# Kernel tuning notes

Hardware: AMD Instinct MI355X
Metric: run time of the kernel (lower is better)

The kernel has to match this reference:

```python
import jax, jax.numpy as jnp
import numpy as np
from jax import lax


def _bilinear_gather(img, ys, xs):
    """img: [B,H,W,C]; ys,xs: [B,K,H,W] fractional coords. Zero padding outside.
    Returns [B,K,H,W,C]."""
    B, H, W, C = img.shape
    y0 = jnp.floor(ys)
    x0 = jnp.floor(xs)
    wy = (ys - y0)[..., None]
    wx = (xs - x0)[..., None]
    y0i = y0.astype(jnp.int32)
    x0i = x0.astype(jnp.int32)
    flat = img.reshape(B, H * W, C)

    def gather(yi, xi):
        valid = (yi >= 0) & (yi < H) & (xi >= 0) & (xi < W)
        yc = jnp.clip(yi, 0, H - 1)
        xc = jnp.clip(xi, 0, W - 1)
        idx = (yc * W + xc).reshape(B, -1, 1)
        g = jnp.take_along_axis(flat, idx, axis=1).reshape(yi.shape + (C,))
        return g * valid[..., None].astype(img.dtype)

    v00 = gather(y0i, x0i)
    v01 = gather(y0i, x0i + 1)
    v10 = gather(y0i + 1, x0i)
    v11 = gather(y0i + 1, x0i + 1)
    one = jnp.asarray(1.0, img.dtype)
    return (v00 * (one - wy) * (one - wx) + v01 * (one - wy) * wx
            + v10 * wy * (one - wx) + v11 * wy * wx)


def _forward(x, w_off, b_off, w_def, b_def, w_attn, b_attn):
    B, Cin, H, W = x.shape
    Cout = w_def.shape[0]
    # offset conv: 3x3, pad 1 -> [B, 18, H, W]
    off = lax.conv_general_dilated(x, w_off, (1, 1), ((1, 1), (1, 1)))
    off = off + b_off[None, :, None, None]
    off = off.reshape(B, 9, 2, H, W)
    dy = off[:, :, 0]  # [B,9,H,W], torchvision order: (dy, dx) per kernel pt
    dx = off[:, :, 1]
    # kernel point grid, row-major over (kh, kw)
    ky, kx = jnp.meshgrid(jnp.arange(3), jnp.arange(3), indexing='ij')
    ky = ky.reshape(9).astype(x.dtype)
    kx = kx.reshape(9).astype(x.dtype)
    ii = jnp.arange(H, dtype=x.dtype)
    jj = jnp.arange(W, dtype=x.dtype)
    # sample position = (out_pos - pad + k) + offset, pad=1, stride=1
    ys = ii[None, None, :, None] - 1.0 + ky[None, :, None, None] + dy
    xs = jj[None, None, None, :] - 1.0 + kx[None, :, None, None] + dx
    img = x.transpose(0, 2, 3, 1)  # [B,H,W,Cin]
    sampled = _bilinear_gather(img, ys, xs)  # [B,9,H,W,Cin]
    wk = w_def.reshape(Cout, Cin, 9)  # row-major kernel pts match ky/kx
    out = jnp.einsum('bkhwc,ock->bohw', sampled, wk) + b_def[None, :, None, None]
    # spatial attention: 1x1 conv -> sigmoid gate
    attn = jnp.einsum('bchw,oc->bohw', out, w_attn[:, :, 0, 0]) + b_attn[None, :, None, None]
    out = out * jax.nn.sigmoid(attn)
    return jax.nn.relu(out)


def setup_inputs() -> dict:
    key = jax.random.key(0)
    ks = jax.random.split(key, 5)
    B, C, H, W = 4, 128, 128, 128
    x = jax.random.normal(ks[0], (B, C, H, W), dtype=jnp.float32)
    w_off = jax.random.normal(ks[1], (18, C, 3, 3), dtype=jnp.float32) * 0.02
    b_off = jnp.zeros((18,), dtype=jnp.float32)
    w_def = jax.random.normal(ks[2], (C, C, 3, 3), dtype=jnp.float32) * (1.0 / np.sqrt(C * 9))
    b_def = jnp.zeros((C,), dtype=jnp.float32)
    w_attn = jax.random.normal(ks[3], (1, C, 1, 1), dtype=jnp.float32) * (1.0 / np.sqrt(C))
    b_attn = jnp.zeros((1,), dtype=jnp.float32)
    return {"x": x, "w_off": w_off, "b_off": b_off, "w_def": w_def,
            "b_def": b_def, "w_attn": w_attn, "b_attn": b_attn}


def reference(x, w_off, b_off, w_def, b_def, w_attn, b_attn):
    return _forward(x, w_off, b_off, w_def, b_def, w_attn, b_attn)
```

## Files before the change

### kernel.cpp

```cpp
#include <hip/hip_runtime.h>
#include <math.h>

#define Cch 128
#define Hh 128
#define Ww 128
#define HW (Hh * Ww)

typedef __attribute__((ext_vector_type(8))) short short8;
typedef __attribute__((ext_vector_type(4))) float float4v;
typedef __attribute__((ext_vector_type(2))) float float2v;
typedef __attribute__((ext_vector_type(4))) unsigned int uint4v;

__device__ __forceinline__ unsigned short f2bf(float f) {
    unsigned u = __float_as_uint(f);
    return (unsigned short)((u + 0x8000u) >> 16);
}
__device__ __forceinline__ float2v up2(unsigned u) {
    return (float2v){__uint_as_float(u << 16), __uint_as_float(u & 0xffff0000u)};
}
__device__ __forceinline__ unsigned packbf2(float lo, float hi) {
    unsigned a = __float_as_uint(lo), b = __float_as_uint(hi);
    return ((a + 0x8000u) >> 16) | ((b + 0x8000u) & 0xffff0000u);
}

__global__ __launch_bounds__(256) void pack_x_v3(const float* __restrict__ x,
                                                 unsigned short* __restrict__ xt) {
    __shared__ unsigned int tile[64][68];
    int t   = threadIdx.x;
    int blk = blockIdx.x;
    int b   = blk >> 8;
    int p0  = (blk & 255) << 6;
    const float* xb = x + (size_t)b * Cch * HW + p0;

    int c2i = t >> 4;
    int q   = t & 15;
    #pragma unroll
    for (int it = 0; it < 4; ++it) {
        int c2 = it * 16 + c2i;
        int px = q * 4;
        float4v a = *(const float4v*)&xb[(size_t)(2 * c2) * HW + px];
        float4v c = *(const float4v*)&xb[(size_t)(2 * c2 + 1) * HW + px];
        #pragma unroll
        for (int j = 0; j < 4; ++j)
            tile[px + j][c2] = packbf2(a[j], c[j]);
    }
    __syncthreads();
    unsigned short* xtb = xt + (size_t)b * HW * Cch + (size_t)p0 * Cch;
    int g  = t & 15;
    int pw = t >> 4;
    #pragma unroll
    for (int it = 0; it < 4; ++it) {
        int p = pw + 16 * it;
        uint4v v = *(const uint4v*)&tile[p][g * 4];
        *(uint4v*)(xtb + (size_t)p * Cch + g * 8) = v;
    }
}

#define NFB (9 * 4 * 8 * 64 * 8)
#define NFO (9 * 4 * 2 * 64 * 8)
__global__ __launch_bounds__(256) void build_frags(const float* __restrict__ w_def,
                                                   const float* __restrict__ w_off,
                                                   unsigned short* __restrict__ wfB,
                                                   unsigned short* __restrict__ wfO) {
    int idx = blockIdx.x * 256 + threadIdx.x;
    if (idx < NFB) {
        int j = idx & 7, lane = (idx >> 3) & 63, t = (idx >> 9) & 7;
        int q = (idx >> 12) & 3, k = idx >> 14;
        int c = 32 * q + 8 * (lane >> 4) + j;
        int o = 16 * t + (lane & 15);
        wfB[idx] = f2bf(w_def[(size_t)(o * Cch + c) * 9 + k]);
    } else if (idx < NFB + NFO) {
        int i2 = idx - NFB;
        int j = i2 & 7, lane = (i2 >> 3) & 63, t = (i2 >> 9) & 1;
        int q = (i2 >> 10) & 3, k = i2 >> 12;
        int c = 32 * q + 8 * (lane >> 4) + j;
        int o = 16 * t + (lane & 15);
        wfO[i2] = (o < 18) ? f2bf(w_off[(size_t)(o * Cch + c) * 9 + k]) : (unsigned short)0;
    }
}

__device__ __forceinline__ void blk_map(int blk, int& b, int& h, int& w0) {
    int xcd = blk & 7;
    b = xcd >> 1;
    int seg = ((xcd & 1) << 8) | (blk >> 3);
    h  = seg >> 2;
    w0 = (seg & 3) << 5;
}

__global__ __launch_bounds__(128, 2) void fused_srt(const unsigned short* __restrict__ xt,
                                                    const unsigned short* __restrict__ wfB,
                                                    const unsigned short* __restrict__ wfO,
                                                    const float* __restrict__ b_off,
                                                    const float* __restrict__ b_def,
                                                    const float* __restrict__ w_attn,
                                                    const float* __restrict__ b_attn,
                                                    float* __restrict__ out) {
    __shared__ float4v red[2 * 8 * 64];
    __shared__ float   offs[32 * 18];
    __shared__ uint4v  smw[2 * 4 * 64];
    int b, h, w0;
    blk_map(blockIdx.x, b, h, w0);
    int tid  = threadIdx.x;
    int wave = tid >> 6;
    int lane = tid & 63;
    int col  = lane & 15;
    int s    = lane >> 4;
    int spx  = lane >> 2;
    int sch  = lane & 3;
    int cbase = 64 * wave;
    int csrt  = cbase + sch * 8;
    int wbase = wave * 256;
    int rIdx  = wbase + ((lane & 15) * 4 + (lane >> 4));

    const unsigned short* xtb = xt + (size_t)b * HW * Cch;

    {
        float4v acc2[2][2];
        #pragma unroll
        for (int pt = 0; pt < 2; ++pt)
            #pragma unroll
            for (int t = 0; t < 2; ++t) {
                int o = 16 * t + col;
                float bv = (wave == 0 && o < 18) ? b_off[o] : 0.0f;
                acc2[pt][t] = (float4v){bv, bv, bv, bv};
            }

        #pragma unroll
        for (int k = 0; k < 9; ++k) {
            int y = h + (k / 3) - 1;
            bool vy = (y >= 0) && (y < Hh);
            int yc = min(max(y, 0), Hh - 1);
            int dxk = (k % 3) - 1;
            int  ofs[2];
            bool val[2];
            #pragma unroll
            for (int pt = 0; pt < 2; ++pt) {
                int px = w0 + 16 * pt + spx;
                int xs = px + dxk;
                val[pt] = vy && (xs >= 0) && (xs < Ww);
                int xc  = min(max(xs, 0), Ww - 1);
                ofs[pt] = (yc * Ww + xc) * Cch + csrt;
            }
            #pragma unroll
            for (int pt = 0; pt < 2; ++pt)
                #pragma unroll
                for (int qq = 0; qq < 2; ++qq) {
                    uint4v av = *(const uint4v*)(xtb + ofs[pt] + 32 * qq);
                    if (!val[pt]) av = (uint4v){0u, 0u, 0u, 0u};
                    smw[wbase + (pt * 2 + qq) * 64 + lane] = av;
                }
            short8 aa[2][2];
            #pragma unroll
            for (int pt = 0; pt < 2; ++pt)
                #pragma unroll
                for (int qq = 0; qq < 2; ++qq)
                    aa[pt][qq] = __builtin_bit_cast(short8, smw[rIdx + (pt * 2 + qq) * 64]);
            #pragma unroll
            for (int qq = 0; qq < 2; ++qq) {
                int q = 2 * wave + qq;
                #pragma unroll
                for (int t = 0; t < 2; ++t) {
                    short8 bv = *(const short8*)(wfO + ((size_t)((k * 4 + q) * 2 + t) * 64 + lane) * 8);
                    #pragma unroll
                    for (int pt = 0; pt < 2; ++pt)
                        acc2[pt][t] = __builtin_amdgcn_mfma_f32_16x16x32_bf16(aa[pt][qq], bv, acc2[pt][t], 0, 0, 0);
                }
            }
        }
        if (wave == 1) {
            #pragma unroll
            for (int pt = 0; pt < 2; ++pt)
                #pragma unroll
                for (int t = 0; t < 2; ++t)
                    red[(pt * 2 + t) * 64 + lane] = acc2[pt][t];
        }
        __syncthreads();
        if (wave == 0) {
            #pragma unroll
            for (int pt = 0; pt < 2; ++pt)
                #pragma unroll
                for (int t = 0; t < 2; ++t) {
                    float4v v = acc2[pt][t] + red[(pt * 2 + t) * 64 + lane];
                    int o = 16 * t + col;
                    if (o < 18) {
                        #pragma unroll
                        for (int r = 0; r < 4; ++r)
                            offs[(16 * pt + 4 * s + r) * 18 + o] = v[r];
                    }
                }
        }
        __syncthreads();
    }

    float4v acc[2][8];
    #pragma unroll
    for (int pt = 0; pt < 2; ++pt)
        #pragma unroll
        for (int t = 0; t < 8; ++t) {
            float bv = (wave == 0) ? b_def[16 * t + col] : 0.0f;
            acc[pt][t] = (float4v){bv, bv, bv, bv};
        }

    int    oaddr[2][4];
    float  wxy[2][4];
    uint4v u[2][8];

#define CALC_TAP(K_) do {                                                    \
    int ky = ((K_) * 11) >> 5;                                               \
    int kx = (K_) - 3 * ky;                                                  \
    _Pragma("unroll")                                                        \
    for (int pt = 0; pt < 2; ++pt) {                                         \
        int pxl = 16 * pt + spx;                                             \
        int px  = w0 + pxl;                                                  \
        float2 dv = *(const float2*)&offs[pxl * 18 + 2 * (K_)];              \
        float ys = (float)(h - 1 + ky) + dv.x;                               \
        float xs = (float)(px - 1 + kx) + dv.y;                              \
        float y0f = floorf(ys), x0f = floorf(xs);                            \
        float wy = ys - y0f, wx = xs - x0f;                                  \
        int y0 = (int)y0f, x0 = (int)x0f;                                    \
        bool vy0 = (y0 >= 0) && (y0 < Hh);                                   \
        bool vy1 = (y0 + 1 >= 0) && (y0 + 1 < Hh);                           \
        bool vx0 = (x0 >= 0) && (x0 < Ww);                                   \
        bool vx1 = (x0 + 1 >= 0) && (x0 + 1 < Ww);                           \
        int y0c = min(max(y0, 0), Hh - 1), y1c = min(max(y0 + 1, 0), Hh - 1);\
        int x0c = min(max(x0, 0), Ww - 1), x1c = min(max(x0 + 1, 0), Ww - 1);\
        wxy[pt][0] = vx0 ? (1.0f - wx) : 0.0f;                               \
        wxy[pt][1] = vx1 ? wx : 0.0f;                                        \
        wxy[pt][2] = vy0 ? (1.0f - wy) : 0.0f;                               \
        wxy[pt][3] = vy1 ? wy : 0.0f;                                        \
        oaddr[pt][0] = (y0c * Ww + x0c) * Cch + csrt;                        \
        oaddr[pt][1] = (y0c * Ww + x1c) * Cch + csrt;                        \
        oaddr[pt][2] = (y1c * Ww + x0c) * Cch + csrt;                        \
        oaddr[pt][3] = (y1c * Ww + x1c) * Cch + csrt;                        \
    }                                                                        \
} while (0)

#define LOAD_TAP() do {                                                      \
    _Pragma("unroll")                                                        \
    for (int pt = 0; pt < 2; ++pt)                                           \
        _Pragma("unroll")                                                    \
        for (int qq = 0; qq < 2; ++qq)                                       \
            _Pragma("unroll")                                                \
            for (int c4 = 0; c4 < 4; ++c4)                                   \
                u[pt][qq * 4 + c4] =                                         \
                    *(const uint4v*)(xtb + oaddr[pt][c4] + 32 * qq);         \
} while (0)

    CALC_TAP(0);
    LOAD_TAP();

    #pragma unroll
    for (int k = 0; k < 9; ++k) {
        const unsigned short* wk = wfB + (size_t)k * 16384 + (size_t)(2 * wave) * 4096;
        short8 bva[8], bvb[8];
        #pragma unroll
        for (int t = 0; t < 8; ++t) {
            bva[t] = *(const short8*)(wk + (size_t)t * 512 + (size_t)lane * 8);
            bvb[t] = *(const short8*)(wk + 4096 + (size_t)t * 512 + (size_t)lane * 8);
        }
        #pragma unroll
        for (int pt = 0; pt < 2; ++pt) {
            float2v A0 = (float2v){wxy[pt][0], wxy[pt][0]};
            float2v A1 = (float2v){wxy[pt][1], wxy[pt][1]};
            float2v B0 = (float2v){wxy[pt][2], wxy[pt][2]};
            float2v B1 = (float2v){wxy[pt][3], wxy[pt][3]};
            #pragma unroll
            for (int qq = 0; qq < 2; ++qq) {
                uint4v res;
                #pragma unroll
                for (int j = 0; j < 4; ++j) {
                    float2v p00 = up2(u[pt][qq * 4 + 0][j]);
                    float2v p01 = up2(u[pt][qq * 4 + 1][j]);
                    float2v p10 = up2(u[pt][qq * 4 + 2][j]);
                    float2v p11 = up2(u[pt][qq * 4 + 3][j]);
                    float2v t0 = __builtin_elementwise_fma(A1, p01, A0 * p00);
                    float2v t1 = __builtin_elementwise_fma(A1, p11, A0 * p10);
                    float2v rr = __builtin_elementwise_fma(B1, t1, B0 * t0);
                    res[j] = packbf2(rr.x, rr.y);
                }
                smw[wbase + (pt * 2 + qq) * 64 + lane] = res;
            }
        }
        if (k < 8) {
            CALC_TAP(k + 1);
            LOAD_TAP();
        }
        short8 afr[2][2];
        #pragma unroll
        for (int pt = 0; pt < 2; ++pt)
            #pragma unroll
            for (int qq = 0; qq < 2; ++qq)
                afr[pt][qq] = __builtin_bit_cast(short8, smw[rIdx + (pt * 2 + qq) * 64]);
        #pragma unroll
        for (int t = 0; t < 8; ++t) {
            acc[0][t] = __builtin_amdgcn_mfma_f32_16x16x32_bf16(afr[0][0], bva[t], acc[0][t], 0, 0, 0);
            acc[1][t] = __builtin_amdgcn_mfma_f32_16x16x32_bf16(afr[1][0], bva[t], acc[1][t], 0, 0, 0);
        }
        #pragma unroll
        for (int t = 0; t < 8; ++t) {
            acc[0][t] = __builtin_amdgcn_mfma_f32_16x16x32_bf16(afr[0][1], bvb[t], acc[0][t], 0, 0, 0);
            acc[1][t] = __builtin_amdgcn_mfma_f32_16x16x32_bf16(afr[1][1], bvb[t], acc[1][t], 0, 0, 0);
        }
    }
#undef CALC_TAP
#undef LOAD_TAP

    if (wave == 1) {
        #pragma unroll
        for (int pt = 0; pt < 2; ++pt)
            #pragma unroll
            for (int t = 0; t < 8; ++t)
                red[(pt * 8 + t) * 64 + lane] = acc[pt][t];
    }
    __syncthreads();
    if (wave == 0) {
        #pragma unroll
        for (int pt = 0; pt < 2; ++pt)
            #pragma unroll
            for (int t = 0; t < 8; ++t)
                acc[pt][t] += red[(pt * 8 + t) * 64 + lane];

        float wA[8];
        #pragma unroll
        for (int t = 0; t < 8; ++t) wA[t] = w_attn[16 * t + col];
        float battn = b_attn[0];
        #pragma unroll
        for (int pt = 0; pt < 2; ++pt) {
            float sig[4];
            #pragma unroll
            for (int r = 0; r < 4; ++r) {
                float pr = 0.0f;
                #pragma unroll
                for (int t = 0; t < 8; ++t) pr = fmaf(acc[pt][t][r], wA[t], pr);
                #pragma unroll
                for (int m = 1; m < 16; m <<= 1) pr += __shfl_xor(pr, m, 64);
                sig[r] = 1.0f / (1.0f + expf(-(pr + battn)));
            }
            #pragma unroll
            for (int t = 0; t < 8; ++t) {
                int o = 16 * t + col;
                float4v v;
                #pragma unroll
                for (int r = 0; r < 4; ++r)
                    v[r] = fmaxf(acc[pt][t][r] * sig[r], 0.0f);
                float* dst = out + ((size_t)(b * Cch + o)) * HW + h * Ww + w0 + 16 * pt + 4 * s;
                *(float4v*)dst = v;
            }
        }
    }
}

extern "C" void kernel_launch(void* const* d_in, const int* in_sizes, int n_in,
                              void* d_out, int out_size, void* d_ws, size_t ws_size,
                              hipStream_t stream) {
    const float* x      = (const float*)d_in[0];
    const float* w_off  = (const float*)d_in[1];
    const float* b_off  = (const float*)d_in[2];
    const float* w_def  = (const float*)d_in[3];
    const float* b_def  = (const float*)d_in[4];
    const float* w_attn = (const float*)d_in[5];
    const float* b_attn = (const float*)d_in[6];
    float* out = (float*)d_out;

    char* ws = (char*)d_ws;
    unsigned short* xt  = (unsigned short*)ws;
    unsigned short* wfB = (unsigned short*)(ws + 16777216);
    unsigned short* wfO = (unsigned short*)(ws + 17072128);

    pack_x_v3<<<1024, 256, 0, stream>>>(x, xt);
    build_frags<<<720, 256, 0, stream>>>(w_def, w_off, wfB, wfO);
    fused_srt<<<2048, 128, 0, stream>>>(xt, wfB, wfO, b_off, b_def, w_attn, b_attn, out);
}
```

Measured before the change: 153.8 us.

## Split pixel halves across four waves instead of two per block

The fused deformable-conv kernel now uses 256 threads per block, four waves instead of two. Each wave owns one 16-pixel half and one channel half, rather than each wave handling both pixel halves. This halves the per-wave accumulators, gather registers and MFMA chains, which cuts register pressure and raises parallelism to hide gather latency. The cost is that each wave now loads the full weight fragments, doubling weight traffic per block.

```diff
diff --git a/kernel.cpp b/kernel.cpp
--- a/kernel.cpp
+++ b/kernel.cpp
@@ -87,43 +87,42 @@
     w0 = (seg & 3) << 5;
 }
 
-__global__ __launch_bounds__(128, 2) void fused_srt(const unsigned short* __restrict__ xt,
-                                                    const unsigned short* __restrict__ wfB,
-                                                    const unsigned short* __restrict__ wfO,
-                                                    const float* __restrict__ b_off,
-                                                    const float* __restrict__ b_def,
-                                                    const float* __restrict__ w_attn,
-                                                    const float* __restrict__ b_attn,
-                                                    float* __restrict__ out) {
+__global__ __launch_bounds__(256, 2) void fused_srt4(const unsigned short* __restrict__ xt,
+                                                     const unsigned short* __restrict__ wfB,
+                                                     const unsigned short* __restrict__ wfO,
+                                                     const float* __restrict__ b_off,
+                                                     const float* __restrict__ b_def,
+                                                     const float* __restrict__ w_attn,
+                                                     const float* __restrict__ b_attn,
+                                                     float* __restrict__ out) {
     __shared__ float4v red[2 * 8 * 64];
     __shared__ float   offs[32 * 18];
-    __shared__ uint4v  smw[2 * 4 * 64];
+    __shared__ uint4v  smw[4 * 2 * 64];
     int b, h, w0;
     blk_map(blockIdx.x, b, h, w0);
-    int tid  = threadIdx.x;
-    int wave = tid >> 6;
-    int lane = tid & 63;
-    int col  = lane & 15;
-    int s    = lane >> 4;
-    int spx  = lane >> 2;
-    int sch  = lane & 3;
-    int cbase = 64 * wave;
-    int csrt  = cbase + sch * 8;
-    int wbase = wave * 256;
+    int tid   = threadIdx.x;
+    int wave  = tid >> 6;
+    int lane  = tid & 63;
+    int pt    = wave & 1;
+    int chalf = wave >> 1;
+    int col   = lane & 15;
+    int s     = lane >> 4;
+    int spx   = lane >> 2;
+    int sch   = lane & 3;
+    int csrt  = 64 * chalf + sch * 8;
+    int wbase = wave * 128;
     int rIdx  = wbase + ((lane & 15) * 4 + (lane >> 4));
 
     const unsigned short* xtb = xt + (size_t)b * HW * Cch;
 
     {
-        float4v acc2[2][2];
-        #pragma unroll
-        for (int pt = 0; pt < 2; ++pt)
-            #pragma unroll
-            for (int t = 0; t < 2; ++t) {
-                int o = 16 * t + col;
-                float bv = (wave == 0 && o < 18) ? b_off[o] : 0.0f;
-                acc2[pt][t] = (float4v){bv, bv, bv, bv};
-            }
+        float4v acc2[2];
+        #pragma unroll
+        for (int t = 0; t < 2; ++t) {
+            int o = 16 * t + col;
+            float bv = (chalf == 0 && o < 18) ? b_off[o] : 0.0f;
+            acc2[t] = (float4v){bv, bv, bv, bv};
+        }
 
         #pragma unroll
         for (int k = 0; k < 9; ++k) {
@@ -131,119 +130,96 @@
             bool vy = (y >= 0) && (y < Hh);
             int yc = min(max(y, 0), Hh - 1);
             int dxk = (k % 3) - 1;
-            int  ofs[2];
-            bool val[2];
-            #pragma unroll
-            for (int pt = 0; pt < 2; ++pt) {
-                int px = w0 + 16 * pt + spx;
-                int xs = px + dxk;
-                val[pt] = vy && (xs >= 0) && (xs < Ww);
-                int xc  = min(max(xs, 0), Ww - 1);
-                ofs[pt] = (yc * Ww + xc) * Cch + csrt;
+            int px = w0 + 16 * pt + spx;
+            int xs = px + dxk;
+            bool val = vy && (xs >= 0) && (xs < Ww);
+            int xc = min(max(xs, 0), Ww - 1);
+            int ofs = (yc * Ww + xc) * Cch + csrt;
+            #pragma unroll
+            for (int qq = 0; qq < 2; ++qq) {
+                uint4v av = *(const uint4v*)(xtb + ofs + 32 * qq);
+                if (!val) av = (uint4v){0u, 0u, 0u, 0u};
+                smw[wbase + qq * 64 + lane] = av;
             }
-            #pragma unroll
-            for (int pt = 0; pt < 2; ++pt)
-                #pragma unroll
-                for (int qq = 0; qq < 2; ++qq) {
-                    uint4v av = *(const uint4v*)(xtb + ofs[pt] + 32 * qq);
-                    if (!val[pt]) av = (uint4v){0u, 0u, 0u, 0u};
-                    smw[wbase + (pt * 2 + qq) * 64 + lane] = av;
-                }
-            short8 aa[2][2];
-            #pragma unroll
-            for (int pt = 0; pt < 2; ++pt)
-                #pragma unroll
-                for (int qq = 0; qq < 2; ++qq)
-                    aa[pt][qq] = __builtin_bit_cast(short8, smw[rIdx + (pt * 2 + qq) * 64]);
+            short8 aa[2];
+            #pragma unroll
+            for (int qq = 0; qq < 2; ++qq)
+                aa[qq] = __builtin_bit_cast(short8, smw[rIdx + qq * 64]);
             #pragma unroll
             for (int qq = 0; qq < 2; ++qq) {
-                int q = 2 * wave + qq;
+                int q = 2 * chalf + qq;
                 #pragma unroll
                 for (int t = 0; t < 2; ++t) {
                     short8 bv = *(const short8*)(wfO + ((size_t)((k * 4 + q) * 2 + t) * 64 + lane) * 8);
-                    #pragma unroll
-                    for (int pt = 0; pt < 2; ++pt)
-                        acc2[pt][t] = __builtin_amdgcn_mfma_f32_16x16x32_bf16(aa[pt][qq], bv, acc2[pt][t], 0, 0, 0);
+                    acc2[t] = __builtin_amdgcn_mfma_f32_16x16x32_bf16(aa[qq], bv, acc2[t], 0, 0, 0);
                 }
             }
         }
-        if (wave == 1) {
-            #pragma unroll
-            for (int pt = 0; pt < 2; ++pt)
-                #pragma unroll
-                for (int t = 0; t < 2; ++t)
-                    red[(pt * 2 + t) * 64 + lane] = acc2[pt][t];
+        if (chalf == 1) {
+            #pragma unroll
+            for (int t = 0; t < 2; ++t)
+                red[(pt * 2 + t) * 64 + lane] = acc2[t];
         }
         __syncthreads();
-        if (wave == 0) {
-            #pragma unroll
-            for (int pt = 0; pt < 2; ++pt)
-                #pragma unroll
-                for (int t = 0; t < 2; ++t) {
-                    float4v v = acc2[pt][t] + red[(pt * 2 + t) * 64 + lane];
-                    int o = 16 * t + col;
-                    if (o < 18) {
-                        #pragma unroll
-                        for (int r = 0; r < 4; ++r)
-                            offs[(16 * pt + 4 * s + r) * 18 + o] = v[r];
-                    }
+        if (chalf == 0) {
+            #pragma unroll
+            for (int t = 0; t < 2; ++t) {
+                float4v v = acc2[t] + red[(pt * 2 + t) * 64 + lane];
+                int o = 16 * t + col;
+                if (o < 18) {
+                    #pragma unroll
+                    for (int r = 0; r < 4; ++r)
+                        offs[(16 * pt + 4 * s + r) * 18 + o] = v[r];
                 }
+            }
         }
         __syncthreads();
     }
 
-    float4v acc[2][8];
+    float4v acc[8];
     #pragma unroll
-    for (int pt = 0; pt < 2; ++pt)
-        #pragma unroll
-        for (int t = 0; t < 8; ++t) {
-            float bv = (wave == 0) ? b_def[16 * t + col] : 0.0f;
-            acc[pt][t] = (float4v){bv, bv, bv, bv};
-        }
-
-    int    oaddr[2][4];
-    float  wxy[2][4];
-    uint4v u[2][8];
+    for (int t = 0; t < 8; ++t) {
+        float bv = (chalf == 0) ? b_def[16 * t + col] : 0.0f;
+        acc[t] = (float4v){bv, bv, bv, bv};
+    }
+
+    int    oaddr[4];
+    float  wxy[4];
+    uint4v u[8];
 
 #define CALC_TAP(K_) do {                                                    \
     int ky = ((K_) * 11) >> 5;                                               \
     int kx = (K_) - 3 * ky;                                                  \
-    _Pragma("unroll")                                                        \
-    for (int pt = 0; pt < 2; ++pt) {                                         \
-        int pxl = 16 * pt + spx;                                             \
-        int px  = w0 + pxl;                                                  \
-        float2 dv = *(const float2*)&offs[pxl * 18 + 2 * (K_)];              \
-        float ys = (float)(h - 1 + ky) + dv.x;                               \
-        float xs = (float)(px - 1 + kx) + dv.y;                              \
-        float y0f = floorf(ys), x0f = floorf(xs);                            \
-        float wy = ys - y0f, wx = xs - x0f;                                  \
-        int y0 = (int)y0f, x0 = (int)x0f;                                    \
-        bool vy0 = (y0 >= 0) && (y0 < Hh);                                   \
-        bool vy1 = (y0 + 1 >= 0) && (y0 + 1 < Hh);                           \
-        bool vx0 = (x0 >= 0) && (x0 < Ww);                                   \
-        bool vx1 = (x0 + 1 >= 0) && (x0 + 1 < Ww);                           \
-        int y0c = min(max(y0, 0), Hh - 1), y1c = min(max(y0 + 1, 0), Hh - 1);\
-        int x0c = min(max(x0, 0), Ww - 1), x1c = min(max(x0 + 1, 0), Ww - 1);\
-        wxy[pt][0] = vx0 ? (1.0f - wx) : 0.0f;                               \
-        wxy[pt][1] = vx1 ? wx : 0.0f;                                        \
-        wxy[pt][2] = vy0 ? (1.0f - wy) : 0.0f;                               \
-        wxy[pt][3] = vy1 ? wy : 0.0f;                                        \
-        oaddr[pt][0] = (y0c * Ww + x0c) * Cch + csrt;                        \
-        oaddr[pt][1] = (y0c * Ww + x1c) * Cch + csrt;                        \
-        oaddr[pt][2] = (y1c * Ww + x0c) * Cch + csrt;                        \
-        oaddr[pt][3] = (y1c * Ww + x1c) * Cch + csrt;                        \
-    }                                                                        \
+    int pxl = 16 * pt + spx;                                                 \
+    int px  = w0 + pxl;                                                      \
+    float2 dv = *(const float2*)&offs[pxl * 18 + 2 * (K_)];                  \
+    float ys = (float)(h - 1 + ky) + dv.x;                                   \
+    float xs = (float)(px - 1 + kx) + dv.y;                                  \
+    float y0f = floorf(ys), x0f = floorf(xs);                                \
+    float wy = ys - y0f, wx = xs - x0f;                                      \
+    int y0 = (int)y0f, x0 = (int)x0f;                                        \
+    bool vy0 = (y0 >= 0) && (y0 < Hh);                                       \
+    bool vy1 = (y0 + 1 >= 0) && (y0 + 1 < Hh);                               \
+    bool vx0 = (x0 >= 0) && (x0 < Ww);                                       \
+    bool vx1 = (x0 + 1 >= 0) && (x0 + 1 < Ww);                               \
+    int y0c = min(max(y0, 0), Hh - 1), y1c = min(max(y0 + 1, 0), Hh - 1);    \
+    int x0c = min(max(x0, 0), Ww - 1), x1c = min(max(x0 + 1, 0), Ww - 1);    \
+    wxy[0] = vx0 ? (1.0f - wx) : 0.0f;                                       \
+    wxy[1] = vx1 ? wx : 0.0f;                                                \
+    wxy[2] = vy0 ? (1.0f - wy) : 0.0f;                                       \
+    wxy[3] = vy1 ? wy : 0.0f;                                                \
+    oaddr[0] = (y0c * Ww + x0c) * Cch + csrt;                                \
+    oaddr[1] = (y0c * Ww + x1c) * Cch + csrt;                                \
+    oaddr[2] = (y1c * Ww + x0c) * Cch + csrt;                                \
+    oaddr[3] = (y1c * Ww + x1c) * Cch + csrt;                                \
 } while (0)
 
 #define LOAD_TAP() do {                                                      \
     _Pragma("unroll")                                                        \
-    for (int pt = 0; pt < 2; ++pt)                                           \
+    for (int qq = 0; qq < 2; ++qq)                                           \
         _Pragma("unroll")                                                    \
-        for (int qq = 0; qq < 2; ++qq)                                       \
-            _Pragma("unroll")                                                \
-            for (int c4 = 0; c4 < 4; ++c4)                                   \
-                u[pt][qq * 4 + c4] =                                         \
-                    *(const uint4v*)(xtb + oaddr[pt][c4] + 32 * qq);         \
+        for (int c4 = 0; c4 < 4; ++c4)                                       \
+            u[qq * 4 + c4] = *(const uint4v*)(xtb + oaddr[c4] + 32 * qq);    \
 } while (0)
 
     CALC_TAP(0);
@@ -251,101 +227,87 @@
 
     #pragma unroll
     for (int k = 0; k < 9; ++k) {
-        const unsigned short* wk = wfB + (size_t)k * 16384 + (size_t)(2 * wave) * 4096;
+        const unsigned short* wk = wfB + (size_t)k * 16384 + (size_t)(2 * chalf) * 4096;
         short8 bva[8], bvb[8];
         #pragma unroll
         for (int t = 0; t < 8; ++t) {
             bva[t] = *(const short8*)(wk + (size_t)t * 512 + (size_t)lane * 8);
             bvb[t] = *(const short8*)(wk + 4096 + (size_t)t * 512 + (size_t)lane * 8);
         }
-        #pragma unroll
-        for (int pt = 0; pt < 2; ++pt) {
-            float2v A0 = (float2v){wxy[pt][0], wxy[pt][0]};
-            float2v A1 = (float2v){wxy[pt][1], wxy[pt][1]};
-            float2v B0 = (float2v){wxy[pt][2], wxy[pt][2]};
-            float2v B1 = (float2v){wxy[pt][3], wxy[pt][3]};
+        {
+            float2v A0 = (float2v){wxy[0], wxy[0]};
+            float2v A1 = (float2v){wxy[1], wxy[1]};
+            float2v B0 = (float2v){wxy[2], wxy[2]};
+            float2v B1 = (float2v){wxy[3], wxy[3]};
             #pragma unroll
             for (int qq = 0; qq < 2; ++qq) {
                 uint4v res;
                 #pragma unroll
                 for (int j = 0; j < 4; ++j) {
-                    float2v p00 = up2(u[pt][qq * 4 + 0][j]);
-                    float2v p01 = up2(u[pt][qq * 4 + 1][j]);
-                    float2v p10 = up2(u[pt][qq * 4 + 2][j]);
-                    float2v p11 = up2(u[pt][qq * 4 + 3][j]);
+                    float2v p00 = up2(u[qq * 4 + 0][j]);
+                    float2v p01 = up2(u[qq * 4 + 1][j]);
+                    float2v p10 = up2(u[qq * 4 + 2][j]);
+                    float2v p11 = up2(u[qq * 4 + 3][j]);
                     float2v t0 = __builtin_elementwise_fma(A1, p01, A0 * p00);
                     float2v t1 = __builtin_elementwise_fma(A1, p11, A0 * p10);
                     float2v rr = __builtin_elementwise_fma(B1, t1, B0 * t0);
                     res[j] = packbf2(rr.x, rr.y);
                 }
-                smw[wbase + (pt * 2 + qq) * 64 + lane] = res;
+                smw[wbase + qq * 64 + lane] = res;
             }
         }
         if (k < 8) {
             CALC_TAP(k + 1);
             LOAD_TAP();
         }
-        short8 afr[2][2];
-        #pragma unroll
-        for (int pt = 0; pt < 2; ++pt)
-            #pragma unroll
-            for (int qq = 0; qq < 2; ++qq)
-                afr[pt][qq] = __builtin_bit_cast(short8, smw[rIdx + (pt * 2 + qq) * 64]);
-        #pragma unroll
-        for (int t = 0; t < 8; ++t) {
-            acc[0][t] = __builtin_amdgcn_mfma_f32_16x16x32_bf16(afr[0][0], bva[t], acc[0][t], 0, 0, 0);
-            acc[1][t] = __builtin_amdgcn_mfma_f32_16x16x32_bf16(afr[1][0], bva[t], acc[1][t], 0, 0, 0);
-        }
-        #pragma unroll
-        for (int t = 0; t < 8; ++t) {
-            acc[0][t] = __builtin_amdgcn_mfma_f32_16x16x32_bf16(afr[0][1], bvb[t], acc[0][t], 0, 0, 0);
-            acc[1][t] = __builtin_amdgcn_mfma_f32_16x16x32_bf16(afr[1][1], bvb[t], acc[1][t], 0, 0, 0);
-        }
+        short8 afr[2];
+        #pragma unroll
+        for (int qq = 0; qq < 2; ++qq)
+            afr[qq] = __builtin_bit_cast(short8, smw[rIdx + qq * 64]);
+        #pragma unroll
+        for (int t = 0; t < 8; ++t)
+            acc[t] = __builtin_amdgcn_mfma_f32_16x16x32_bf16(afr[0], bva[t], acc[t], 0, 0, 0);
+        #pragma unroll
+        for (int t = 0; t < 8; ++t)
+            acc[t] = __builtin_amdgcn_mfma_f32_16x16x32_bf16(afr[1], bvb[t], acc[t], 0, 0, 0);
     }
 #undef CALC_TAP
 #undef LOAD_TAP
 
-    if (wave == 1) {
-        #pragma unroll
-        for (int pt = 0; pt < 2; ++pt)
-            #pragma unroll
-            for (int t = 0; t < 8; ++t)
-                red[(pt * 8 + t) * 64 + lane] = acc[pt][t];
+    if (chalf == 1) {
+        #pragma unroll
+        for (int t = 0; t < 8; ++t)
+            red[(pt * 8 + t) * 64 + lane] = acc[t];
     }
     __syncthreads();
-    if (wave == 0) {
-        #pragma unroll
-        for (int pt = 0; pt < 2; ++pt)
-            #pragma unroll
-            for (int t = 0; t < 8; ++t)
-                acc[pt][t] += red[(pt * 8 + t) * 64 + lane];
+    if (chalf == 0) {
+        #pragma unroll
+        for (int t = 0; t < 8; ++t)
+            acc[t] += red[(pt * 8 + t) * 64 + lane];
 
         float wA[8];
         #pragma unroll
         for (int t = 0; t < 8; ++t) wA[t] = w_attn[16 * t + col];
         float battn = b_attn[0];
-        #pragma unroll
-        for (int pt = 0; pt < 2; ++pt) {
-            float sig[4];
-            #pragma unroll
-            for (int r = 0; r < 4; ++r) {
-                float pr = 0.0f;
-                #pragma unroll
-                for (int t = 0; t < 8; ++t) pr = fmaf(acc[pt][t][r], wA[t], pr);
-                #pragma unroll
-                for (int m = 1; m < 16; m <<= 1) pr += __shfl_xor(pr, m, 64);
-                sig[r] = 1.0f / (1.0f + expf(-(pr + battn)));
-            }
-            #pragma unroll
-            for (int t = 0; t < 8; ++t) {
-                int o = 16 * t + col;
-                float4v v;
-                #pragma unroll
-                for (int r = 0; r < 4; ++r)
-                    v[r] = fmaxf(acc[pt][t][r] * sig[r], 0.0f);
-                float* dst = out + ((size_t)(b * Cch + o)) * HW + h * Ww + w0 + 16 * pt + 4 * s;
-                *(float4v*)dst = v;
-            }
+        float sig[4];
+        #pragma unroll
+        for (int r = 0; r < 4; ++r) {
+            float pr = 0.0f;
+            #pragma unroll
+            for (int t = 0; t < 8; ++t) pr = fmaf(acc[t][r], wA[t], pr);
+            #pragma unroll
+            for (int m = 1; m < 16; m <<= 1) pr += __shfl_xor(pr, m, 64);
+            sig[r] = 1.0f / (1.0f + expf(-(pr + battn)));
+        }
+        #pragma unroll
+        for (int t = 0; t < 8; ++t) {
+            int o = 16 * t + col;
+            float4v v;
+            #pragma unroll
+            for (int r = 0; r < 4; ++r)
+                v[r] = fmaxf(acc[t][r] * sig[r], 0.0f);
+            float* dst = out + ((size_t)(b * Cch + o)) * HW + h * Ww + w0 + 16 * pt + 4 * s;
+            *(float4v*)dst = v;
         }
     }
 }
@@ -369,5 +331,5 @@
 
     pack_x_v3<<<1024, 256, 0, stream>>>(x, xt);
     build_frags<<<720, 256, 0, stream>>>(w_def, w_off, wfB, wfO);
-    fused_srt<<<2048, 128, 0, stream>>>(xt, wfB, wfO, b_off, b_def, w_attn, b_attn, out);
-}
+    fused_srt4<<<2048, 256, 0, stream>>>(xt, wfB, wfO, b_off, b_def, w_attn, b_attn, out);
+}
```

Measured after the change: 169.9 us. +10.5%, slower.
